# Kernel optimization log

Hardware: AMD Instinct MI355X
Metric: run time of the kernel (lower is better)

The kernel has to match this reference:

```python
import jax, jax.numpy as jnp
import numpy as np

D, H, DH = 64, 4, 32
INNER = H * DH
SCALE = 1.0 / np.sqrt(DH)


def _layernorm(x, w, b, eps=1e-5):
    mu = jnp.mean(x, axis=-1, keepdims=True)
    var = jnp.var(x, axis=-1, keepdims=True)
    return (x - mu) * jax.lax.rsqrt(var + eps) * w + b


def setup_inputs() -> dict:
    key = jax.random.key(0)
    ks = jax.random.split(key, 8)
    B, N = 1, 256
    z = jax.random.normal(ks[0], (B, N, N, D), dtype=jnp.float32)
    mask = jax.random.randint(ks[1], (B, N, N), 0, 2).astype(jnp.bool_)
    ln_w = jnp.ones((D,), jnp.float32)
    ln_b = jnp.zeros((D,), jnp.float32)
    w_qkv = jax.random.normal(ks[2], (3 * INNER, D), jnp.float32) * 0.02
    w_bias = jax.random.normal(ks[3], (H, D), jnp.float32) * 0.02
    w_out = jax.random.normal(ks[4], (D, INNER), jnp.float32) * 0.02
    w_gate = jax.random.normal(ks[5], (INNER, D), jnp.float32) * 0.02
    return {"z": z, "mask": mask, "ln_w": ln_w, "ln_b": ln_b,
            "w_qkv": w_qkv, "w_bias": w_bias, "w_out": w_out, "w_gate": w_gate}


def reference(z, mask, ln_w, ln_b, w_qkv, w_bias, w_out, w_gate):
    # mode == 'starting': attend along the second pair axis per row n.
    B, N = z.shape[0], z.shape[1]
    h = _layernorm(z, ln_w, ln_b)                       # [B,N,N,D]
    qkv = jnp.einsum('bijd,ed->bije', h, w_qkv)         # [B,N,N,3*INNER]
    qkv = qkv.reshape(B, N, N, 3, H, DH)
    q, k, v = qkv[..., 0, :, :], qkv[..., 1, :, :], qkv[..., 2, :, :]  # [B,N,N,H,dh]
    attn = jnp.einsum('bnihd,bnjhd->bnhij', q, k) * SCALE  # [B,N,H,N,N]
    bias = jnp.einsum('bijd,hd->bhij', h, w_bias)          # [B,H,N,N]
    attn = attn + bias[:, None]                            # broadcast over n
    big_neg = jnp.finfo(attn.dtype).min
    attn = jnp.where(mask[:, :, None, None, :], attn, big_neg)  # mask keys j per (b,n)
    attn = jax.nn.softmax(attn, axis=-1)
    out = jnp.einsum('bnhij,bnjhd->bnihd', attn, v)        # [B,N,N,H,dh]
    out = out.reshape(B, N, N, INNER)
    gate = jax.nn.sigmoid(jnp.einsum('bijd,ed->bije', h, w_gate))
    out = jnp.einsum('bije,de->bijd', out * gate, w_out)
    return out
```

## Files before the change

kernel.cpp:

```cpp
#include <hip/hip_runtime.h>
#include <hip/hip_bf16.h>

#define N_ 256
#define D_ 64
#define H_ 4
#define DH_ 32
#define EQKV 384
#define EGATE 128
#define NPOS 65536
#define SCALE_F 0.17677669529663687f
#define BIG_NEG -3.402823466e38f
#define P_STRIDE 264
#define H_STRIDE 72
#define X_STRIDE 136

typedef __attribute__((ext_vector_type(8))) short s16x8;
typedef __attribute__((ext_vector_type(4))) float f32x4;


__device__ inline short bfbits(float x) {
    __hip_bfloat16 b = __float2bfloat16(x);
    return *reinterpret_cast<short*>(&b);
}
__device__ inline float b2f(short s) {
    unsigned u = ((unsigned)(unsigned short)s) << 16;
    union { unsigned u; float f; } c; c.u = u; return c.f;
}
__device__ inline s16x8 cvt8(float4 a, float4 b) {
    s16x8 r;
    r[0] = bfbits(a.x); r[1] = bfbits(a.y); r[2] = bfbits(a.z); r[3] = bfbits(a.w);
    r[4] = bfbits(b.x); r[5] = bfbits(b.y); r[6] = bfbits(b.z); r[7] = bfbits(b.w);
    return r;
}

__global__ __launch_bounds__(512) void k1_ln_proj_mfma(
    const float* __restrict__ z, const float* __restrict__ ln_w, const float* __restrict__ ln_b,
    const float* __restrict__ w_qkv, const float* __restrict__ w_gate, const float* __restrict__ w_bias,
    __hip_bfloat16* __restrict__ qkv_ws, float* __restrict__ gate_ws, float* __restrict__ bias_ws)
{
    __shared__ short h_bf[64 * H_STRIDE];
    const int t = threadIdx.x;
    const int wave = t >> 6, lane = t & 63;
    const int pos0 = blockIdx.x * 64;
    const int m = lane & 15, quad = lane >> 4;

    {
        const float lw = ln_w[lane], lb = ln_b[lane];
        const float wb0 = w_bias[lane], wb1 = w_bias[64 + lane],
                    wb2 = w_bias[128 + lane], wb3 = w_bias[192 + lane];
        for (int pp = 0; pp < 8; ++pp) {
            const int p = wave * 8 + pp;
            const float zv = z[(size_t)(pos0 + p) * 64 + lane];
            float s = zv, s2 = zv * zv;
            #pragma unroll
            for (int off = 32; off; off >>= 1) { s += __shfl_xor(s, off); s2 += __shfl_xor(s2, off); }
            const float mu = s * 0.015625f;
            const float var = s2 * 0.015625f - mu * mu;
            const float rs = rsqrtf(var + 1e-5f);
            const float hv = (zv - mu) * rs * lw + lb;
            h_bf[p * H_STRIDE + lane] = bfbits(hv);
            float b0 = hv * wb0, b1 = hv * wb1, b2 = hv * wb2, b3 = hv * wb3;
            #pragma unroll
            for (int off = 32; off; off >>= 1) {
                b0 += __shfl_xor(b0, off); b1 += __shfl_xor(b1, off);
                b2 += __shfl_xor(b2, off); b3 += __shfl_xor(b3, off);
            }
            if (lane < 4) {
                const int gpos = pos0 + p;
                const int gi = gpos >> 8, gj = gpos & 255;
                const float bv = lane == 0 ? b0 : lane == 1 ? b1 : lane == 2 ? b2 : b3;
                bias_ws[lane * NPOS + gi * 256 + gj] = bv;
            }
        }
    }
    __syncthreads();

    const int colbase = wave * 64;
    s16x8 bfrag[4][2];
    #pragma unroll
    for (int nt = 0; nt < 4; ++nt) {
        const int col = colbase + nt * 16 + m;
        const float* wp = (col < EQKV) ? (w_qkv + (size_t)col * 64)
                                       : (w_gate + (size_t)(col - EQKV) * 64);
        #pragma unroll
        for (int kt = 0; kt < 2; ++kt) {
            const float4 w0 = *(const float4*)(wp + kt * 32 + quad * 8);
            const float4 w1 = *(const float4*)(wp + kt * 32 + quad * 8 + 4);
            bfrag[nt][kt] = cvt8(w0, w1);
        }
    }

    s16x8 afrag[4][2];
    #pragma unroll
    for (int mt = 0; mt < 4; ++mt)
        #pragma unroll
        for (int kt = 0; kt < 2; ++kt)
            afrag[mt][kt] = *(const s16x8*)(h_bf + (mt * 16 + m) * H_STRIDE + kt * 32 + quad * 8);

    f32x4 acc[4][4];
    #pragma unroll
    for (int mt = 0; mt < 4; ++mt)
        #pragma unroll
        for (int nt = 0; nt < 4; ++nt)
            acc[mt][nt] = (f32x4){0.f, 0.f, 0.f, 0.f};

    #pragma unroll
    for (int kt = 0; kt < 2; ++kt)
        #pragma unroll
        for (int mt = 0; mt < 4; ++mt)
            #pragma unroll
            for (int nt = 0; nt < 4; ++nt)
                acc[mt][nt] = __builtin_amdgcn_mfma_f32_16x16x32_bf16(
                    afrag[mt][kt], bfrag[nt][kt], acc[mt][nt], 0, 0, 0);

    if (colbase < EQKV) {
        #pragma unroll
        for (int mt = 0; mt < 4; ++mt)
            #pragma unroll
            for (int nt = 0; nt < 4; ++nt) {
                const int c = colbase + nt * 16 + m;
                #pragma unroll
                for (int r = 0; r < 4; ++r) {
                    const int p = pos0 + mt * 16 + quad * 4 + r;
                    qkv_ws[(size_t)p * EQKV + c] = __float2bfloat16(acc[mt][nt][r]);
                }
            }
    } else {
        #pragma unroll
        for (int mt = 0; mt < 4; ++mt)
            #pragma unroll
            for (int nt = 0; nt < 4; ++nt) {
                const int c = colbase - EQKV + nt * 16 + m;
                #pragma unroll
                for (int r = 0; r < 4; ++r) {
                    const int p = pos0 + mt * 16 + quad * 4 + r;
                    gate_ws[(size_t)p * EGATE + c] = 1.0f / (1.0f + __expf(-acc[mt][nt][r]));
                }
            }
    }
}

__global__ __launch_bounds__(512, 4) void k2_attn_mfma(
    const __hip_bfloat16* __restrict__ qkv_ws, const float* __restrict__ bias_ws,
    const int* __restrict__ mask, __hip_bfloat16* __restrict__ attn_bf)
{
    __shared__ short p_s[64 * P_STRIDE];
    __shared__ short vt_s[32 * P_STRIDE];
    __shared__ float keep[256];
    __shared__ float redm[64][2];
    __shared__ float redl[64][2];

    const int bx = blockIdx.x;
    const int n = bx & 255, h = bx >> 8;
    const int t = threadIdx.x;
    const int wave = t >> 6, lane = t & 63;
    const int m = lane & 15, quad = lane >> 4;
    const int mt = wave & 3, nh = wave >> 2;

    if (t < 256) keep[t] = (mask[n * 256 + t] != 0) ? 1.0f : 0.0f;

    {
        const int j = t >> 1, dh = (t & 1) * 16;
        const __hip_bfloat16* vp = qkv_ws + (size_t)(n * 256 + j) * 384 + 256 + h * 32 + dh;
        s16x8 v0 = *(const s16x8*)vp;
        s16x8 v1 = *(const s16x8*)(vp + 8);
        #pragma unroll
        for (int e = 0; e < 8; ++e) {
            vt_s[(dh + e) * P_STRIDE + j]     = v0[e];
            vt_s[(dh + 8 + e) * P_STRIDE + j] = v1[e];
        }
    }

    s16x8 kf[8];
    #pragma unroll
    for (int tt = 0; tt < 8; ++tt) {
        const int jt = nh * 8 + tt;
        kf[tt] = *(const s16x8*)(qkv_ws + (size_t)(n * 256 + jt * 16 + m) * 384 + 128 + h * 32 + quad * 8);
    }
    __syncthreads();

    for (int ig = 0; ig < 4; ++ig) {
        const int i0 = ig * 64;

        f32x4 s[8];
        {
            const size_t qbase = (size_t)(n * 256 + i0 + mt * 16 + m) * 384 + h * 32 + quad * 8;
            const s16x8 afrag = *(const s16x8*)(qkv_ws + qbase);
            #pragma unroll
            for (int tt = 0; tt < 8; ++tt) {
                f32x4 z4 = {0.f, 0.f, 0.f, 0.f};
                s[tt] = __builtin_amdgcn_mfma_f32_16x16x32_bf16(afrag, kf[tt], z4, 0, 0, 0);
            }
        }
        #pragma unroll
        for (int tt = 0; tt < 8; ++tt) {
            const int j = (nh * 8 + tt) * 16 + m;
            const float kp = keep[j];
            const float* bp = bias_ws + (size_t)h * NPOS + j;
            #pragma unroll
            for (int r = 0; r < 4; ++r) {
                const int irow = i0 + mt * 16 + quad * 4 + r;
                const float sv = s[tt][r] * SCALE_F + bp[irow * 256];
                s[tt][r] = (kp != 0.f) ? sv : BIG_NEG;
            }
        }
        {
            float mp[4];
            #pragma unroll
            for (int r = 0; r < 4; ++r) {
                float v = s[0][r];
                #pragma unroll
                for (int tt = 1; tt < 8; ++tt) v = fmaxf(v, s[tt][r]);
                #pragma unroll
                for (int off = 1; off < 16; off <<= 1) v = fmaxf(v, __shfl_xor(v, off));
                mp[r] = v;
            }
            if (m == 0) {
                #pragma unroll
                for (int r = 0; r < 4; ++r) redm[mt * 16 + quad * 4 + r][nh] = mp[r];
            }
        }
        __syncthreads();

        {
            float ls[4];
            #pragma unroll
            for (int r = 0; r < 4; ++r) {
                const int row = mt * 16 + quad * 4 + r;
                const float gm = fmaxf(redm[row][0], redm[row][1]);
                float acc = 0.f;
                #pragma unroll
                for (int tt = 0; tt < 8; ++tt) {
                    const float p = __expf(s[tt][r] - gm);
                    s[tt][r] = p;
                    acc += p;
                }
                #pragma unroll
                for (int off = 1; off < 16; off <<= 1) acc += __shfl_xor(acc, off);
                ls[r] = acc;
            }
            if (m == 0) {
                #pragma unroll
                for (int r = 0; r < 4; ++r) redl[mt * 16 + quad * 4 + r][nh] = ls[r];
            }
            #pragma unroll
            for (int tt = 0; tt < 8; ++tt) {
                const int col = (nh * 8 + tt) * 16 + m;
                #pragma unroll
                for (int r = 0; r < 4; ++r) {
                    const int row = mt * 16 + quad * 4 + r;
                    p_s[row * P_STRIDE + col] = bfbits(s[tt][r]);
                }
            }
        }
        __syncthreads();

        {
            f32x4 o = {0.f, 0.f, 0.f, 0.f};
            const int arow = mt * 16 + m;
            const int brow = nh * 16 + m;
            #pragma unroll
            for (int kt = 0; kt < 8; ++kt) {
                const s16x8 ap = *(const s16x8*)(p_s + arow * P_STRIDE + kt * 32 + quad * 8);
                const s16x8 bv = *(const s16x8*)(vt_s + brow * P_STRIDE + kt * 32 + quad * 8);
                o = __builtin_amdgcn_mfma_f32_16x16x32_bf16(ap, bv, o, 0, 0, 0);
            }
            #pragma unroll
            for (int r = 0; r < 4; ++r) {
                const int row = mt * 16 + quad * 4 + r;
                const float l = redl[row][0] + redl[row][1];
                const float val = o[r] * (1.0f / l);
                const int ig_row = i0 + row;
                attn_bf[(size_t)(n * 256 + ig_row) * 128 + h * 32 + nh * 16 + m] = __float2bfloat16(val);
            }
        }
        __syncthreads();
    }
}

__global__ __launch_bounds__(512) void k3_proj_mfma(
    const __hip_bfloat16* __restrict__ attn_bf, const float* __restrict__ gate_ws,
    const float* __restrict__ w_out, float* __restrict__ out)
{
    __shared__ short x_bf[64 * X_STRIDE];
    const int t = threadIdx.x;
    const int wave = t >> 6, lane = t & 63;
    const int pos0 = blockIdx.x * 64;
    const int m = lane & 15, quad = lane >> 4;
    const int mt = wave & 3, nh = wave >> 2;

    #pragma unroll
    for (int r = 0; r < 4; ++r) {
        const int idx = r * 512 + t;
        const int p = idx >> 5;
        const int c4 = (idx & 31) * 4;
        const size_t g = (size_t)(pos0 + p) * 128 + c4;
        const short4 ab = *(const short4*)(attn_bf + g);
        const float4 gt = *(const float4*)(gate_ws + g);
        short4 sv;
        sv.x = bfbits(b2f(ab.x) * gt.x); sv.y = bfbits(b2f(ab.y) * gt.y);
        sv.z = bfbits(b2f(ab.z) * gt.z); sv.w = bfbits(b2f(ab.w) * gt.w);
        *(short4*)(x_bf + p * X_STRIDE + c4) = sv;
    }
    __syncthreads();

    s16x8 bfrag[2][4];
    #pragma unroll
    for (int nt = 0; nt < 2; ++nt) {
        const int d = nh * 32 + nt * 16 + m;
        const float* wp = w_out + (size_t)d * 128;
        #pragma unroll
        for (int kt = 0; kt < 4; ++kt) {
            const float4 w0 = *(const float4*)(wp + kt * 32 + quad * 8);
            const float4 w1 = *(const float4*)(wp + kt * 32 + quad * 8 + 4);
            bfrag[nt][kt] = cvt8(w0, w1);
        }
    }

    s16x8 afrag[4];
    #pragma unroll
    for (int kt = 0; kt < 4; ++kt)
        afrag[kt] = *(const s16x8*)(x_bf + (mt * 16 + m) * X_STRIDE + kt * 32 + quad * 8);

    f32x4 acc[2];
    acc[0] = (f32x4){0.f, 0.f, 0.f, 0.f};
    acc[1] = (f32x4){0.f, 0.f, 0.f, 0.f};
    #pragma unroll
    for (int kt = 0; kt < 4; ++kt) {
        acc[0] = __builtin_amdgcn_mfma_f32_16x16x32_bf16(afrag[kt], bfrag[0][kt], acc[0], 0, 0, 0);
        acc[1] = __builtin_amdgcn_mfma_f32_16x16x32_bf16(afrag[kt], bfrag[1][kt], acc[1], 0, 0, 0);
    }

    #pragma unroll
    for (int nt = 0; nt < 2; ++nt) {
        const int d = nh * 32 + nt * 16 + m;
        #pragma unroll
        for (int r = 0; r < 4; ++r) {
            const int p = pos0 + mt * 16 + quad * 4 + r;
            out[(size_t)p * 64 + d] = acc[nt][r];
        }
    }
}

extern "C" void kernel_launch(void* const* d_in, const int* in_sizes, int n_in,
                              void* d_out, int out_size, void* d_ws, size_t ws_size,
                              hipStream_t stream) {
    const float* z      = (const float*)d_in[0];
    const int*   mask   = (const int*)d_in[1];
    const float* ln_w   = (const float*)d_in[2];
    const float* ln_b   = (const float*)d_in[3];
    const float* w_qkv  = (const float*)d_in[4];
    const float* w_bias = (const float*)d_in[5];
    const float* w_out  = (const float*)d_in[6];
    const float* w_gate = (const float*)d_in[7];
    float* out = (float*)d_out;

    char* ws = (char*)d_ws;
    __hip_bfloat16* qkv_ws  = (__hip_bfloat16*)(ws);
    float*          bias_ws = (float*)(ws + 50331648);
    float*          gate_ws = (float*)(ws + 51380224);
    __hip_bfloat16* attn_bf = (__hip_bfloat16*)(ws + 84934656);

    k1_ln_proj_mfma<<<1024, 512, 0, stream>>>(z, ln_w, ln_b, w_qkv, w_gate, w_bias,
                                              qkv_ws, gate_ws, bias_ws);
    k2_attn_mfma<<<1024, 512, 0, stream>>>(qkv_ws, bias_ws, mask, attn_bf);
    k3_proj_mfma<<<1024, 512, 0, stream>>>(attn_bf, gate_ws, w_out, out);
}
```

Before: 204.1 us.

## Move gate projection into output kernel and stage global stores through LDS

The gate projection and sigmoid move from the first kernel into the projection kernel. The first kernel now writes a bf16 copy of the normalized activations instead of an fp32 gate tensor, which cuts workspace traffic. The qkv and output stores are staged through shared memory so each global write is a wide, coalesced vector store instead of a scattered scalar store. This adds extra LDS use and barriers, and the gate matmul is recomputed in the third kernel.

```diff
diff --git a/kernel.cpp b/kernel.cpp
--- a/kernel.cpp
+++ b/kernel.cpp
@@ -6,13 +6,15 @@
 #define H_ 4
 #define DH_ 32
 #define EQKV 384
-#define EGATE 128
 #define NPOS 65536
 #define SCALE_F 0.17677669529663687f
 #define BIG_NEG -3.402823466e38f
 #define P_STRIDE 264
 #define H_STRIDE 72
 #define X_STRIDE 136
+#define A_STRIDE 136
+#define O_STRIDE 68
+#define Q_STRIDE 392
 
 typedef __attribute__((ext_vector_type(8))) short s16x8;
 typedef __attribute__((ext_vector_type(4))) float f32x4;
@@ -35,10 +37,11 @@
 
 __global__ __launch_bounds__(512) void k1_ln_proj_mfma(
     const float* __restrict__ z, const float* __restrict__ ln_w, const float* __restrict__ ln_b,
-    const float* __restrict__ w_qkv, const float* __restrict__ w_gate, const float* __restrict__ w_bias,
-    __hip_bfloat16* __restrict__ qkv_ws, float* __restrict__ gate_ws, float* __restrict__ bias_ws)
+    const float* __restrict__ w_qkv, const float* __restrict__ w_bias,
+    __hip_bfloat16* __restrict__ qkv_ws, __hip_bfloat16* __restrict__ h_ws,
+    float* __restrict__ bias_ws)
 {
-    __shared__ short h_bf[64 * H_STRIDE];
+    __shared__ __align__(16) short smem[64 * Q_STRIDE];
     const int t = threadIdx.x;
     const int wave = t >> 6, lane = t & 63;
     const int pos0 = blockIdx.x * 64;
@@ -58,7 +61,7 @@
             const float var = s2 * 0.015625f - mu * mu;
             const float rs = rsqrtf(var + 1e-5f);
             const float hv = (zv - mu) * rs * lw + lb;
-            h_bf[p * H_STRIDE + lane] = bfbits(hv);
+            smem[p * H_STRIDE + lane] = bfbits(hv);
             float b0 = hv * wb0, b1 = hv * wb1, b2 = hv * wb2, b3 = hv * wb3;
             #pragma unroll
             for (int off = 32; off; off >>= 1) {
@@ -75,13 +78,18 @@
     }
     __syncthreads();
 
-    const int colbase = wave * 64;
-    s16x8 bfrag[4][2];
-    #pragma unroll
-    for (int nt = 0; nt < 4; ++nt) {
+    {
+        const int row = t >> 3, c8 = (t & 7) * 8;
+        *(s16x8*)(h_ws + (size_t)(pos0 + row) * 64 + c8) =
+            *(const s16x8*)(smem + row * H_STRIDE + c8);
+    }
+
+    const int colbase = wave * 48;
+    s16x8 bfrag[3][2];
+    #pragma unroll
+    for (int nt = 0; nt < 3; ++nt) {
         const int col = colbase + nt * 16 + m;
-        const float* wp = (col < EQKV) ? (w_qkv + (size_t)col * 64)
-                                       : (w_gate + (size_t)(col - EQKV) * 64);
+        const float* wp = w_qkv + (size_t)col * 64;
         #pragma unroll
         for (int kt = 0; kt < 2; ++kt) {
             const float4 w0 = *(const float4*)(wp + kt * 32 + quad * 8);
@@ -95,13 +103,13 @@
     for (int mt = 0; mt < 4; ++mt)
         #pragma unroll
         for (int kt = 0; kt < 2; ++kt)
-            afrag[mt][kt] = *(const s16x8*)(h_bf + (mt * 16 + m) * H_STRIDE + kt * 32 + quad * 8);
-
-    f32x4 acc[4][4];
+            afrag[mt][kt] = *(const s16x8*)(smem + (mt * 16 + m) * H_STRIDE + kt * 32 + quad * 8);
+
+    f32x4 acc[4][3];
     #pragma unroll
     for (int mt = 0; mt < 4; ++mt)
         #pragma unroll
-        for (int nt = 0; nt < 4; ++nt)
+        for (int nt = 0; nt < 3; ++nt)
             acc[mt][nt] = (f32x4){0.f, 0.f, 0.f, 0.f};
 
     #pragma unroll
@@ -109,34 +117,31 @@
         #pragma unroll
         for (int mt = 0; mt < 4; ++mt)
             #pragma unroll
-            for (int nt = 0; nt < 4; ++nt)
+            for (int nt = 0; nt < 3; ++nt)
                 acc[mt][nt] = __builtin_amdgcn_mfma_f32_16x16x32_bf16(
                     afrag[mt][kt], bfrag[nt][kt], acc[mt][nt], 0, 0, 0);
 
-    if (colbase < EQKV) {
-        #pragma unroll
-        for (int mt = 0; mt < 4; ++mt)
-            #pragma unroll
-            for (int nt = 0; nt < 4; ++nt) {
-                const int c = colbase + nt * 16 + m;
-                #pragma unroll
-                for (int r = 0; r < 4; ++r) {
-                    const int p = pos0 + mt * 16 + quad * 4 + r;
-                    qkv_ws[(size_t)p * EQKV + c] = __float2bfloat16(acc[mt][nt][r]);
-                }
-            }
-    } else {
-        #pragma unroll
-        for (int mt = 0; mt < 4; ++mt)
-            #pragma unroll
-            for (int nt = 0; nt < 4; ++nt) {
-                const int c = colbase - EQKV + nt * 16 + m;
-                #pragma unroll
-                for (int r = 0; r < 4; ++r) {
-                    const int p = pos0 + mt * 16 + quad * 4 + r;
-                    gate_ws[(size_t)p * EGATE + c] = 1.0f / (1.0f + __expf(-acc[mt][nt][r]));
-                }
-            }
+    __syncthreads();
+
+    #pragma unroll
+    for (int mt = 0; mt < 4; ++mt)
+        #pragma unroll
+        for (int nt = 0; nt < 3; ++nt) {
+            const int c = colbase + nt * 16 + m;
+            #pragma unroll
+            for (int r = 0; r < 4; ++r) {
+                const int row = mt * 16 + quad * 4 + r;
+                smem[row * Q_STRIDE + c] = bfbits(acc[mt][nt][r]);
+            }
+        }
+    __syncthreads();
+
+    #pragma unroll
+    for (int i = 0; i < 6; ++i) {
+        const int idx = i * 512 + t;
+        const int row = idx / 48, c8 = (idx % 48) * 8;
+        *(s16x8*)(qkv_ws + (size_t)(pos0 + row) * EQKV + c8) =
+            *(const s16x8*)(smem + row * Q_STRIDE + c8);
     }
 }
 
@@ -144,8 +149,8 @@
     const __hip_bfloat16* __restrict__ qkv_ws, const float* __restrict__ bias_ws,
     const int* __restrict__ mask, __hip_bfloat16* __restrict__ attn_bf)
 {
-    __shared__ short p_s[64 * P_STRIDE];
-    __shared__ short vt_s[32 * P_STRIDE];
+    __shared__ __align__(16) short p_s[64 * P_STRIDE];
+    __shared__ __align__(16) short vt_s[32 * P_STRIDE];
     __shared__ float keep[256];
     __shared__ float redm[64][2];
     __shared__ float redl[64][2];
@@ -279,31 +284,59 @@
 }
 
 __global__ __launch_bounds__(512) void k3_proj_mfma(
-    const __hip_bfloat16* __restrict__ attn_bf, const float* __restrict__ gate_ws,
-    const float* __restrict__ w_out, float* __restrict__ out)
+    const __hip_bfloat16* __restrict__ attn_bf, const __hip_bfloat16* __restrict__ h_ws,
+    const float* __restrict__ w_gate, const float* __restrict__ w_out, float* __restrict__ out)
 {
-    __shared__ short x_bf[64 * X_STRIDE];
+    __shared__ __align__(16) short h_s[64 * H_STRIDE];
+    __shared__ __align__(16) short a_s[64 * A_STRIDE];
+    __shared__ __align__(16) short x_s[64 * X_STRIDE];
     const int t = threadIdx.x;
     const int wave = t >> 6, lane = t & 63;
     const int pos0 = blockIdx.x * 64;
     const int m = lane & 15, quad = lane >> 4;
+
+    {
+        const int row = t >> 3, c8 = (t & 7) * 8;
+        *(s16x8*)(h_s + row * H_STRIDE + c8) =
+            *(const s16x8*)(h_ws + (size_t)(pos0 + row) * 64 + c8);
+    }
+    #pragma unroll
+    for (int i = 0; i < 2; ++i) {
+        const int idx = i * 512 + t;
+        const int row = idx >> 4, c8 = (idx & 15) * 8;
+        *(s16x8*)(a_s + row * A_STRIDE + c8) =
+            *(const s16x8*)(attn_bf + (size_t)(pos0 + row) * 128 + c8);
+    }
+    __syncthreads();
+
+    {
+        const int mt = wave & 3, cg = wave >> 2;
+        s16x8 ha[2];
+        #pragma unroll
+        for (int kt = 0; kt < 2; ++kt)
+            ha[kt] = *(const s16x8*)(h_s + (mt * 16 + m) * H_STRIDE + kt * 32 + quad * 8);
+        #pragma unroll
+        for (int nt = 0; nt < 4; ++nt) {
+            const float* wp = w_gate + (size_t)(cg * 64 + nt * 16 + m) * 64;
+            const s16x8 b0 = cvt8(*(const float4*)(wp + quad * 8),
+                                  *(const float4*)(wp + quad * 8 + 4));
+            const s16x8 b1 = cvt8(*(const float4*)(wp + 32 + quad * 8),
+                                  *(const float4*)(wp + 32 + quad * 8 + 4));
+            f32x4 g4 = (f32x4){0.f, 0.f, 0.f, 0.f};
+            g4 = __builtin_amdgcn_mfma_f32_16x16x32_bf16(ha[0], b0, g4, 0, 0, 0);
+            g4 = __builtin_amdgcn_mfma_f32_16x16x32_bf16(ha[1], b1, g4, 0, 0, 0);
+            const int col = cg * 64 + nt * 16 + m;
+            #pragma unroll
+            for (int r = 0; r < 4; ++r) {
+                const int row = mt * 16 + quad * 4 + r;
+                const float gv = 1.0f / (1.0f + __expf(-g4[r]));
+                x_s[row * X_STRIDE + col] = bfbits(b2f(a_s[row * A_STRIDE + col]) * gv);
+            }
+        }
+    }
+    __syncthreads();
+
     const int mt = wave & 3, nh = wave >> 2;
-
-    #pragma unroll
-    for (int r = 0; r < 4; ++r) {
-        const int idx = r * 512 + t;
-        const int p = idx >> 5;
-        const int c4 = (idx & 31) * 4;
-        const size_t g = (size_t)(pos0 + p) * 128 + c4;
-        const short4 ab = *(const short4*)(attn_bf + g);
-        const float4 gt = *(const float4*)(gate_ws + g);
-        short4 sv;
-        sv.x = bfbits(b2f(ab.x) * gt.x); sv.y = bfbits(b2f(ab.y) * gt.y);
-        sv.z = bfbits(b2f(ab.z) * gt.z); sv.w = bfbits(b2f(ab.w) * gt.w);
-        *(short4*)(x_bf + p * X_STRIDE + c4) = sv;
-    }
-    __syncthreads();
-
     s16x8 bfrag[2][4];
     #pragma unroll
     for (int nt = 0; nt < 2; ++nt) {
@@ -320,7 +353,7 @@
     s16x8 afrag[4];
     #pragma unroll
     for (int kt = 0; kt < 4; ++kt)
-        afrag[kt] = *(const s16x8*)(x_bf + (mt * 16 + m) * X_STRIDE + kt * 32 + quad * 8);
+        afrag[kt] = *(const s16x8*)(x_s + (mt * 16 + m) * X_STRIDE + kt * 32 + quad * 8);
 
     f32x4 acc[2];
     acc[0] = (f32x4){0.f, 0.f, 0.f, 0.f};
@@ -331,14 +364,24 @@
         acc[1] = __builtin_amdgcn_mfma_f32_16x16x32_bf16(afrag[kt], bfrag[1][kt], acc[1], 0, 0, 0);
     }
 
+    float* o_s = (float*)a_s;
     #pragma unroll
     for (int nt = 0; nt < 2; ++nt) {
         const int d = nh * 32 + nt * 16 + m;
         #pragma unroll
         for (int r = 0; r < 4; ++r) {
-            const int p = pos0 + mt * 16 + quad * 4 + r;
-            out[(size_t)p * 64 + d] = acc[nt][r];
-        }
+            const int row = mt * 16 + quad * 4 + r;
+            o_s[row * O_STRIDE + d] = acc[nt][r];
+        }
+    }
+    __syncthreads();
+
+    #pragma unroll
+    for (int i = 0; i < 2; ++i) {
+        const int idx = i * 512 + t;
+        const int row = idx >> 4, c4 = (idx & 15) * 4;
+        *(float4*)(out + (size_t)(pos0 + row) * 64 + c4) =
+            *(const float4*)(o_s + row * O_STRIDE + c4);
     }
 }
 
@@ -358,11 +401,11 @@
     char* ws = (char*)d_ws;
     __hip_bfloat16* qkv_ws  = (__hip_bfloat16*)(ws);
     float*          bias_ws = (float*)(ws + 50331648);
-    float*          gate_ws = (float*)(ws + 51380224);
-    __hip_bfloat16* attn_bf = (__hip_bfloat16*)(ws + 84934656);
-
-    k1_ln_proj_mfma<<<1024, 512, 0, stream>>>(z, ln_w, ln_b, w_qkv, w_gate, w_bias,
-                                              qkv_ws, gate_ws, bias_ws);
+    __hip_bfloat16* h_ws    = (__hip_bfloat16*)(ws + 51380224);
+    __hip_bfloat16* attn_bf = (__hip_bfloat16*)(ws + 59768832);
+
+    k1_ln_proj_mfma<<<1024, 512, 0, stream>>>(z, ln_w, ln_b, w_qkv, w_bias,
+                                              qkv_ws, h_ws, bias_ws);
     k2_attn_mfma<<<1024, 512, 0, stream>>>(qkv_ws, bias_ws, mask, attn_bf);
-    k3_proj_mfma<<<1024, 512, 0, stream>>>(attn_bf, gate_ws, w_out, out);
-}
+    k3_proj_mfma<<<1024, 512, 0, stream>>>(attn_bf, h_ws, w_gate, w_out, out);
+}
```

Measured after the change: 202.9 us. About the same (-0.6%).
